# Optimization experiments

Hardware: AMD Instinct MI355X
Metric: run time of the kernel (lower is better)

Reference implementation:

```python
import jax, jax.numpy as jnp
import numpy as np

B, M, D = 64, 2048, 512


def setup_inputs() -> dict:
    key = jax.random.key(0)
    k1, k2 = jax.random.split(key)
    inputs = jax.random.normal(k1, (B, D), dtype=jnp.float32)
    buffer = jax.random.normal(k2, (B, M, D), dtype=jnp.float32)
    return {"inputs": inputs, "buffer": buffer}


def reference(inputs, buffer):
    # inputs: [B, D]; buffer: [B, M, D]
    # Faithful to the torch eval path: per-row L2 distance to each stored
    # pattern, then argMAX (as in the original code), then gather.
    diff = buffer - inputs[:, None, :]              # [B, M, D]
    dist = jnp.linalg.norm(diff, axis=-1)           # [B, M]
    idx = jnp.argmax(dist, axis=-1)                 # [B]
    recalled = jnp.take_along_axis(buffer, idx[:, None, None], axis=1)  # [B, 1, D]
    return recalled[:, 0, :]                        # [B, D]
```

## Files before the change

kernel.cpp:

```cpp
#include <hip/hip_runtime.h>

#define BB 64
#define MM 2048
#define DD 512
#define CHUNK 64
#define SPLITS (MM / CHUNK)

__global__ __launch_bounds__(256) void dist_argmax_kernel(
    const float* __restrict__ inputs,
    const float* __restrict__ buffer,
    float* __restrict__ ws_d,
    int*   __restrict__ ws_i)
{
    const int b     = blockIdx.x;
    const int chunk = blockIdx.y;
    const int tid   = threadIdx.x;
    const int lane  = tid & 63;
    const int wave  = tid >> 6;
    const int g     = lane >> 4;
    const int j     = lane & 15;

    const float4* q4 = (const float4*)(inputs + (size_t)b * DD);
    float4 q[8];
    #pragma unroll
    for (int k = 0; k < 8; k++) q[k] = q4[j + k * 16];

    const float* base =
        buffer + (size_t)b * MM * DD + (size_t)chunk * CHUNK * DD;

    float best_d = -1.0f;
    int   best_i = 0;

    #pragma unroll
    for (int p = 0; p < 4; p++) {
        const int r = wave * 16 + p * 4 + g;
        const float4* row4 = (const float4*)(base + (size_t)r * DD);
        float s = 0.0f;
        #pragma unroll
        for (int k = 0; k < 8; k++) {
            float4 v = row4[j + k * 16];
            float dx;
            dx = v.x - q[k].x; s = fmaf(dx, dx, s);
            dx = v.y - q[k].y; s = fmaf(dx, dx, s);
            dx = v.z - q[k].z; s = fmaf(dx, dx, s);
            dx = v.w - q[k].w; s = fmaf(dx, dx, s);
        }
        #pragma unroll
        for (int off = 1; off < 16; off <<= 1)
            s += __shfl_xor(s, off, 64);
        if (s > best_d) { best_d = s; best_i = r; }
    }

    #pragma unroll
    for (int off = 16; off < 64; off <<= 1) {
        float od = __shfl_xor(best_d, off, 64);
        int   oi = __shfl_xor(best_i, off, 64);
        if (od > best_d || (od == best_d && oi < best_i)) {
            best_d = od; best_i = oi;
        }
    }

    __shared__ float sd[4];
    __shared__ int   si[4];
    if (lane == 0) { sd[wave] = best_d; si[wave] = best_i; }
    __syncthreads();
    if (tid == 0) {
        float bd = sd[0]; int bi = si[0];
        #pragma unroll
        for (int w = 1; w < 4; w++) {
            if (sd[w] > bd || (sd[w] == bd && si[w] < bi)) { bd = sd[w]; bi = si[w]; }
        }
        ws_d[b * SPLITS + chunk] = bd;
        ws_i[b * SPLITS + chunk] = chunk * CHUNK + bi;
    }
}

__global__ __launch_bounds__(128) void gather_kernel(
    const float* __restrict__ ws_d,
    const int*   __restrict__ ws_i,
    const float* __restrict__ buffer,
    float*       __restrict__ out)
{
    const int b   = blockIdx.x;
    const int tid = threadIdx.x;
    __shared__ int s_idx;

    if (tid < 64) {
        float d = (tid < SPLITS) ? ws_d[b * SPLITS + tid] : -1.0f;
        int   i = (tid < SPLITS) ? ws_i[b * SPLITS + tid] : 0x7fffffff;
        #pragma unroll
        for (int off = 32; off > 0; off >>= 1) {
            float od = __shfl_down(d, off, 64);
            int   oi = __shfl_down(i, off, 64);
            if (od > d || (od == d && oi < i)) { d = od; i = oi; }
        }
        if (tid == 0) s_idx = i;
    }
    __syncthreads();

    const int idx = s_idx;
    const float4* src = (const float4*)(buffer + ((size_t)b * MM + idx) * DD);
    float4*       dst = (float4*)(out + (size_t)b * DD);
    dst[tid] = src[tid];
}

extern "C" void kernel_launch(void* const* d_in, const int* in_sizes, int n_in,
                              void* d_out, int out_size, void* d_ws, size_t ws_size,
                              hipStream_t stream) {
    const float* inputs = (const float*)d_in[0];
    const float* buffer = (const float*)d_in[1];
    float* out  = (float*)d_out;
    float* ws_d = (float*)d_ws;
    int*   ws_i = (int*)(ws_d + BB * SPLITS);

    dim3 grid(BB, SPLITS);
    dist_argmax_kernel<<<grid, 256, 0, stream>>>(inputs, buffer, ws_d, ws_i);
    gather_kernel<<<BB, 128, 0, stream>>>(ws_d, ws_i, buffer, out);
}
```

Before: 403.9 us.

## Fuse gather into distance kernel via packed atomicMax and last-block election

Removes the separate gather kernel. Each block packs its best distance and inverted index into a 64-bit word and merges it with atomicMax. A completion counter then elects the last block per batch row, which reads the winner and copies the row to the output. This saves a kernel launch and its dependency gap, at the cost of a memset launch, per-block atomics and a threadfence.

```diff
diff --git a/kernel.cpp b/kernel.cpp
--- a/kernel.cpp
+++ b/kernel.cpp
@@ -6,11 +6,12 @@
 #define CHUNK 64
 #define SPLITS (MM / CHUNK)
 
-__global__ __launch_bounds__(256) void dist_argmax_kernel(
+__global__ __launch_bounds__(256) void knn_fused_kernel(
     const float* __restrict__ inputs,
     const float* __restrict__ buffer,
-    float* __restrict__ ws_d,
-    int*   __restrict__ ws_i)
+    unsigned long long* __restrict__ ws_best,
+    unsigned int* __restrict__ ws_cnt,
+    float* __restrict__ out)
 {
     const int b     = blockIdx.x;
     const int chunk = blockIdx.y;
@@ -62,46 +63,37 @@
 
     __shared__ float sd[4];
     __shared__ int   si[4];
+    __shared__ int   s_gather;
     if (lane == 0) { sd[wave] = best_d; si[wave] = best_i; }
     __syncthreads();
+
     if (tid == 0) {
         float bd = sd[0]; int bi = si[0];
         #pragma unroll
         for (int w = 1; w < 4; w++) {
             if (sd[w] > bd || (sd[w] == bd && si[w] < bi)) { bd = sd[w]; bi = si[w]; }
         }
-        ws_d[b * SPLITS + chunk] = bd;
-        ws_i[b * SPLITS + chunk] = chunk * CHUNK + bi;
-    }
-}
-
-__global__ __launch_bounds__(128) void gather_kernel(
-    const float* __restrict__ ws_d,
-    const int*   __restrict__ ws_i,
-    const float* __restrict__ buffer,
-    float*       __restrict__ out)
-{
-    const int b   = blockIdx.x;
-    const int tid = threadIdx.x;
-    __shared__ int s_idx;
-
-    if (tid < 64) {
-        float d = (tid < SPLITS) ? ws_d[b * SPLITS + tid] : -1.0f;
-        int   i = (tid < SPLITS) ? ws_i[b * SPLITS + tid] : 0x7fffffff;
-        #pragma unroll
-        for (int off = 32; off > 0; off >>= 1) {
-            float od = __shfl_down(d, off, 64);
-            int   oi = __shfl_down(i, off, 64);
-            if (od > d || (od == d && oi < i)) { d = od; i = oi; }
+        const unsigned gidx = (unsigned)(chunk * CHUNK + bi);
+        const unsigned long long pack =
+            ((unsigned long long)__float_as_uint(bd) << 32) | (0xFFFFFFFFu - gidx);
+        atomicMax(ws_best + b, pack);
+        __threadfence();
+        const unsigned prev = atomicAdd(ws_cnt + b, 1u);
+        if (prev == SPLITS - 1) {
+            const unsigned long long v = atomicMax(ws_best + b, 0ULL);
+            s_gather = (int)(0xFFFFFFFFu - (unsigned)(v & 0xFFFFFFFFu));
+        } else {
+            s_gather = -1;
         }
-        if (tid == 0) s_idx = i;
     }
     __syncthreads();
 
-    const int idx = s_idx;
-    const float4* src = (const float4*)(buffer + ((size_t)b * MM + idx) * DD);
-    float4*       dst = (float4*)(out + (size_t)b * DD);
-    dst[tid] = src[tid];
+    const int idx = s_gather;
+    if (idx >= 0 && tid < 128) {
+        const float4* src = (const float4*)(buffer + ((size_t)b * MM + idx) * DD);
+        float4*       dst = (float4*)(out + (size_t)b * DD);
+        dst[tid] = src[tid];
+    }
 }
 
 extern "C" void kernel_launch(void* const* d_in, const int* in_sizes, int n_in,
@@ -109,11 +101,14 @@
                               hipStream_t stream) {
     const float* inputs = (const float*)d_in[0];
     const float* buffer = (const float*)d_in[1];
-    float* out  = (float*)d_out;
-    float* ws_d = (float*)d_ws;
-    int*   ws_i = (int*)(ws_d + BB * SPLITS);
+    float* out = (float*)d_out;
+
+    unsigned long long* ws_best = (unsigned long long*)d_ws;
+    unsigned int*       ws_cnt  = (unsigned int*)(ws_best + BB);
+
+    hipMemsetAsync(d_ws, 0, BB * sizeof(unsigned long long) + BB * sizeof(unsigned int),
+                   stream);
 
     dim3 grid(BB, SPLITS);
-    dist_argmax_kernel<<<grid, 256, 0, stream>>>(inputs, buffer, ws_d, ws_i);
-    gather_kernel<<<BB, 128, 0, stream>>>(ws_d, ws_i, buffer, out);
+    knn_fused_kernel<<<grid, 256, 0, stream>>>(inputs, buffer, ws_best, ws_cnt, out);
 }
```

After: 479.8 us. 18.8% more time.

## Stage buffer rows through double-buffered LDS with async global-to-LDS copies

Applied to the files above, without the earlier changes.

Each block now streams its 64-row chunk as eight 8-row tiles, copied into a double-buffered LDS region with `global_load_lds` while the previous tile is being reduced. The goal is to overlap memory fetch with the distance computation. Threads are remapped to 32 lanes per row, each handling 16 contiguous floats, and the per-thread LDS read order is rotated to spread bank accesses. In exchange it adds a block barrier per tile and keeps far fewer loads in flight per thread than the fully unrolled direct-load version. Correctness relies on the barrier also waiting for the async copies to finish.

```diff
diff --git a/kernel.cpp b/kernel.cpp
--- a/kernel.cpp
+++ b/kernel.cpp
@@ -1,10 +1,21 @@
 #include <hip/hip_runtime.h>
+#include <stdint.h>
 
 #define BB 64
 #define MM 2048
 #define DD 512
 #define CHUNK 64
 #define SPLITS (MM / CHUNK)
+#define TROWS 8
+#define NT (CHUNK / TROWS)
+#define TILE_FLOATS (TROWS * DD)
+#define TILE_BYTES (TILE_FLOATS * 4)
+
+__device__ __forceinline__ void async_copy16(const void* g, void* l) {
+    __builtin_amdgcn_global_load_lds(
+        (const __attribute__((address_space(1))) unsigned int*)g,
+        (__attribute__((address_space(3))) unsigned int*)l, 16, 0, 0);
+}
 
 __global__ __launch_bounds__(256) void dist_argmax_kernel(
     const float* __restrict__ inputs,
@@ -12,33 +23,54 @@
     float* __restrict__ ws_d,
     int*   __restrict__ ws_i)
 {
+    __shared__ float lds[2 * TILE_FLOATS];
+    __shared__ float sd[4];
+    __shared__ int   si[4];
+
     const int b     = blockIdx.x;
     const int chunk = blockIdx.y;
     const int tid   = threadIdx.x;
     const int lane  = tid & 63;
     const int wave  = tid >> 6;
-    const int g     = lane >> 4;
-    const int j     = lane & 15;
+    const int c     = tid & 31;
+    const int rit   = tid >> 5;
 
-    const float4* q4 = (const float4*)(inputs + (size_t)b * DD);
-    float4 q[8];
+    const float4* q4 = (const float4*)(inputs + (size_t)b * DD + (size_t)c * 16);
+    float4 q[4];
     #pragma unroll
-    for (int k = 0; k < 8; k++) q[k] = q4[j + k * 16];
+    for (int k = 0; k < 4; k++) q[k] = q4[k];
 
-    const float* base =
-        buffer + (size_t)b * MM * DD + (size_t)chunk * CHUNK * DD;
+    const char* gbase = (const char*)(buffer + (size_t)b * MM * DD
+                                             + (size_t)chunk * CHUNK * DD);
+    char* lbase = (char*)lds;
+
+    #pragma unroll
+    for (int i = 0; i < 4; i++)
+        async_copy16(gbase + (size_t)i * 4096 + (size_t)tid * 16,
+                     lbase + (size_t)i * 4096 + (size_t)tid * 16);
 
     float best_d = -1.0f;
     int   best_i = 0;
 
-    #pragma unroll
-    for (int p = 0; p < 4; p++) {
-        const int r = wave * 16 + p * 4 + g;
-        const float4* row4 = (const float4*)(base + (size_t)r * DD);
+    for (int t = 0; t < NT; t++) {
+        __syncthreads();
+
+        if (t + 1 < NT) {
+            const char* g = gbase + (size_t)(t + 1) * TILE_BYTES;
+            char*       l = lbase + (size_t)((t + 1) & 1) * TILE_BYTES;
+            #pragma unroll
+            for (int i = 0; i < 4; i++)
+                async_copy16(g + (size_t)i * 4096 + (size_t)tid * 16,
+                             l + (size_t)i * 4096 + (size_t)tid * 16);
+        }
+
+        const float* L = lds + (size_t)(t & 1) * TILE_FLOATS
+                             + (size_t)rit * DD + (size_t)c * 16;
         float s = 0.0f;
         #pragma unroll
-        for (int k = 0; k < 8; k++) {
-            float4 v = row4[j + k * 16];
+        for (int k0 = 0; k0 < 4; k0++) {
+            const int k = (k0 + (c >> 1)) & 3;
+            float4 v = *(const float4*)(L + k * 4);
             float dx;
             dx = v.x - q[k].x; s = fmaf(dx, dx, s);
             dx = v.y - q[k].y; s = fmaf(dx, dx, s);
@@ -46,22 +78,20 @@
             dx = v.w - q[k].w; s = fmaf(dx, dx, s);
         }
         #pragma unroll
-        for (int off = 1; off < 16; off <<= 1)
+        for (int off = 1; off < 32; off <<= 1)
             s += __shfl_xor(s, off, 64);
+
+        const int r = chunk * CHUNK + t * TROWS + rit;
         if (s > best_d) { best_d = s; best_i = r; }
     }
 
-    #pragma unroll
-    for (int off = 16; off < 64; off <<= 1) {
-        float od = __shfl_xor(best_d, off, 64);
-        int   oi = __shfl_xor(best_i, off, 64);
+    {
+        float od = __shfl_xor(best_d, 32, 64);
+        int   oi = __shfl_xor(best_i, 32, 64);
         if (od > best_d || (od == best_d && oi < best_i)) {
             best_d = od; best_i = oi;
         }
     }
-
-    __shared__ float sd[4];
-    __shared__ int   si[4];
     if (lane == 0) { sd[wave] = best_d; si[wave] = best_i; }
     __syncthreads();
     if (tid == 0) {
@@ -71,7 +101,7 @@
             if (sd[w] > bd || (sd[w] == bd && si[w] < bi)) { bd = sd[w]; bi = si[w]; }
         }
         ws_d[b * SPLITS + chunk] = bd;
-        ws_i[b * SPLITS + chunk] = chunk * CHUNK + bi;
+        ws_i[b * SPLITS + chunk] = bi;
     }
 }
 
```

After: 374.6 us. 7.3% less time.
